# Optimization experiments

Hardware: AMD Instinct MI355X
Metric: run time of the kernel (lower is better)

The kernel has to match this reference:

```python
import jax, jax.numpy as jnp
import numpy as np

N = 50000
E = 500000
D = 128      # input_nf = output_nf = hidden_nf
EPS = 1e-8
MAX_TRANS = 10.0


def setup_inputs() -> dict:
    key = jax.random.key(0)
    ks = jax.random.split(key, 16)
    s = lambda k, shp: jax.random.normal(k, shp, dtype=jnp.float32) * 0.05
    inp = {
        "h": jax.random.normal(ks[0], (N, D), dtype=jnp.float32),
        "edge_index": jax.random.randint(ks[1], (2, E), 0, N, dtype=jnp.int64),
        "coord": jax.random.normal(ks[2], (N, 3), dtype=jnp.float32),
        # edge_mlp: Linear(2D+1 -> D), SiLU, Linear(D -> D), SiLU
        "We1": s(ks[3], (2 * D + 1, D)), "be1": jnp.zeros((D,), jnp.float32),
        "We2": s(ks[4], (D, D)),         "be2": jnp.zeros((D,), jnp.float32),
        # att_mlp: Linear(D -> 1), Sigmoid
        "Watt": s(ks[5], (D, 1)), "batt": jnp.zeros((1,), jnp.float32),
        # coord_mlp: Linear(D -> D), SiLU, Linear(D -> 1, bias=False, xavier gain=0.001)
        "Wc1": s(ks[6], (D, D)), "bc1": jnp.zeros((D,), jnp.float32),
        "Wc2": s(ks[7], (D, 1)) * 0.001,
        # node_mlp: Linear(2D -> D), SiLU, Linear(D -> D)
        "Wn1": s(ks[8], (2 * D, D)), "bn1": jnp.zeros((D,), jnp.float32),
        "Wn2": s(ks[9], (D, D)),     "bn2": jnp.zeros((D,), jnp.float32),
    }
    return inp


def _segment_mean(data, seg_ids, num_segments):
    tot = jax.ops.segment_sum(data, seg_ids, num_segments=num_segments)
    cnt = jax.ops.segment_sum(jnp.ones_like(data), seg_ids, num_segments=num_segments)
    return tot / jnp.clip(cnt, 1.0, None)


def reference(h, edge_index, coord, We1, be1, We2, be2, Watt, batt,
              Wc1, bc1, Wc2, Wn1, bn1, Wn2, bn2):
    row, col = edge_index[0], edge_index[1]

    # coord2radial (normalize=False)
    coord_diff = coord[row] - coord[col]                      # [E, 3]
    radial = jnp.sum(coord_diff ** 2, axis=1, keepdims=True)  # [E, 1]

    # edge_model with attention
    e_in = jnp.concatenate([h[row], h[col], radial], axis=1)  # [E, 2D+1]
    e = jax.nn.silu(e_in @ We1 + be1)
    edge_feat = jax.nn.silu(e @ We2 + be2)                    # [E, D]
    att = jax.nn.sigmoid(edge_feat @ Watt + batt)             # [E, 1]
    edge_feat = edge_feat * att

    # coord_model (update_coords=True, coords_agg='mean', tanh=False)
    cw = jax.nn.silu(edge_feat @ Wc1 + bc1) @ Wc2             # [E, 1]
    trans = jnp.clip(coord_diff * cw, -MAX_TRANS, MAX_TRANS)  # [E, 3]
    agg_c = jnp.clip(_segment_mean(trans, row, N), -MAX_TRANS, MAX_TRANS)
    coord_out = coord + agg_c

    # node_model (residual=True)
    agg = jax.ops.segment_sum(edge_feat, row, num_segments=N)  # [N, D]
    n_in = jnp.concatenate([h, agg], axis=1)                   # [N, 2D]
    h_out = h + (jax.nn.silu(n_in @ Wn1 + bn1) @ Wn2 + bn2)

    return h_out, coord_out, edge_feat
```

## Files before the change

### kernel.cpp

```cpp
#include <hip/hip_runtime.h>

typedef unsigned short ushort_t;
typedef __attribute__((ext_vector_type(8))) short short8;
typedef __attribute__((ext_vector_type(4))) short short4v;
typedef __attribute__((ext_vector_type(4))) float f32x4;

#define NN 50000
#define EE 500000
#define DD 128
#define MAXT 10.0f

#define MFMA(a,b,c) __builtin_amdgcn_mfma_f32_16x16x32_bf16((a),(b),(c),0,0,0)

__device__ __forceinline__ ushort_t f2bf(float x){
  unsigned u = __float_as_uint(x);
  u += 0x7FFFu + ((u>>16)&1u);
  return (ushort_t)(u>>16);
}
__device__ __forceinline__ float sigm(float x){ return 1.0f/(1.0f+__expf(-x)); }
__device__ __forceinline__ float siluf(float x){ return x*sigm(x); }
__device__ __forceinline__ float clamp10(float x){ return fminf(fmaxf(x,-MAXT),MAXT); }

__global__ void k_prep(const float* __restrict__ We1, const float* __restrict__ We2,
                       const float* __restrict__ Wc1, const float* __restrict__ Wn1,
                       const float* __restrict__ Wn2, ushort_t* __restrict__ wpre)
{
  int idx = blockIdx.x*256 + threadIdx.x;
  if (idx >= 7*16384) return;
  int mat = idx >> 14;
  int loc = idx & 16383;
  int n = loc >> 7;
  int kidx = loc & 127;
  int ko = 16*(kidx&7) + (kidx>>3);
  float v;
  switch(mat){
    case 0: v = We1[kidx*DD + n]; break;
    case 1: v = We1[(128+kidx)*DD + n]; break;
    case 2: v = We2[ko*DD + n]; break;
    case 3: v = Wc1[ko*DD + n]; break;
    case 4: v = Wn1[kidx*DD + n]; break;
    case 5: v = Wn1[(128+kidx)*DD + n]; break;
    default: v = Wn2[ko*DD + n]; break;
  }
  int byteoff = n*256 + ((kidx*2) ^ ((n&7)<<4));
  *(ushort_t*)((char*)wpre + (size_t)mat*32768 + byteoff) = f2bf(v);
}

__global__ void k_hprep(const float* __restrict__ h, ushort_t* __restrict__ hb)
{
  int i = blockIdx.x*256 + threadIdx.x;
  if (i >= NN*DD/8) return;
  f32x4 x = ((const f32x4*)h)[2*i];
  f32x4 y = ((const f32x4*)h)[2*i+1];
  short8 t;
  #pragma unroll
  for (int j=0;j<4;++j){ t[j]=(short)f2bf(x[j]); t[j+4]=(short)f2bf(y[j]); }
  ((short8*)hb)[i] = t;
}

__global__ void k_zero(int* __restrict__ cnt){
  int i = blockIdx.x*256 + threadIdx.x;
  if (i < NN) cnt[i] = 0;
}
__global__ void k_count(const int* __restrict__ eidx, int* __restrict__ cnt){
  int e = blockIdx.x*256 + threadIdx.x;
  if (e < EE) atomicAdd(&cnt[eidx[e]], 1);
}
#define SCAN_B 196
__global__ void k_bsum(const int* __restrict__ cnt, int* __restrict__ bsum){
  __shared__ int sh[256];
  int t = threadIdx.x;
  int i = blockIdx.x*256 + t;
  sh[t] = (i < NN) ? cnt[i] : 0;
  __syncthreads();
  for (int off=128; off>0; off>>=1){
    if (t < off) sh[t] += sh[t+off];
    __syncthreads();
  }
  if (t==0) bsum[blockIdx.x] = sh[0];
}
__global__ void k_bscan(const int* __restrict__ bsum, int* __restrict__ boff){
  __shared__ int sh[256];
  int t = threadIdx.x;
  sh[t] = (t < SCAN_B) ? bsum[t] : 0;
  __syncthreads();
  for (int off=1; off<256; off<<=1){
    int x = (t>=off) ? sh[t-off] : 0;
    __syncthreads();
    sh[t] += x;
    __syncthreads();
  }
  if (t < SCAN_B) boff[t] = (t>0) ? sh[t-1] : 0;
}
__global__ void k_rscan(const int* __restrict__ cnt, const int* __restrict__ boff,
                        int* __restrict__ rowstart, int* __restrict__ cursor){
  __shared__ int sh[256];
  int t = threadIdx.x;
  int i = blockIdx.x*256 + t;
  int v = (i < NN) ? cnt[i] : 0;
  sh[t] = v;
  __syncthreads();
  for (int off=1; off<256; off<<=1){
    int x = (t>=off) ? sh[t-off] : 0;
    __syncthreads();
    sh[t] += x;
    __syncthreads();
  }
  int excl = sh[t] - v + boff[blockIdx.x];
  if (i < NN){ rowstart[i] = excl; cursor[i] = excl; }
  if (i == 0) rowstart[NN] = EE;
}
__global__ void k_scatter(const int* __restrict__ eidx, int* __restrict__ cursor,
                          int* __restrict__ csr){
  int e = blockIdx.x*256 + threadIdx.x;
  if (e < EE){
    int p = atomicAdd(&cursor[eidx[e]], 1);
    csr[p] = e;
  }
}

__device__ __forceinline__ void stage(const ushort_t* __restrict__ wpre, int mat,
                                      ushort_t* Wbuf, int tid)
{
  const f32x4* src = (const f32x4*)(wpre + (size_t)mat*16384);
  f32x4* dst = (f32x4*)Wbuf;
  #pragma unroll
  for (int i=0;i<4;++i) dst[tid + 512*i] = src[tid + 512*i];
}
__device__ __forceinline__ void zacc(f32x4 acc[2][4]){
  #pragma unroll
  for (int i=0;i<2;++i)
    #pragma unroll
    for (int j=0;j<4;++j) acc[i][j] = (f32x4){0.f,0.f,0.f,0.f};
}
__device__ __forceinline__ void gemm_b16(const short8 af[2][4], const ushort_t* Wbuf,
                                         int cbase, int q, int s, f32x4 acc[2][4])
{
  #pragma unroll
  for (int kc=0;kc<4;++kc){
    const int koff = ((kc*64+q*16) ^ ((s&7)<<4));
    #pragma unroll
    for (int ct=0;ct<4;++ct){
      short8 bf = *(const short8*)((const char*)Wbuf + (cbase+ct*16+s)*256 + koff);
      acc[0][ct] = MFMA(af[0][kc],bf,acc[0][ct]);
      acc[1][ct] = MFMA(af[1][kc],bf,acc[1][ct]);
    }
  }
}
__device__ __forceinline__ void gemm_lds16(const ushort_t* ebuf, const ushort_t* Wbuf,
                                           int mbase, int cbase, int q, int s,
                                           f32x4 acc[2][4])
{
  #pragma unroll
  for (int kc=0;kc<4;++kc){
    const int koff = ((kc*64+q*16) ^ ((s&7)<<4));
    short8 a0 = *(const short8*)((const char*)ebuf + (mbase+s)*256 + koff);
    short8 a1 = *(const short8*)((const char*)ebuf + (mbase+16+s)*256 + koff);
    #pragma unroll
    for (int ct=0;ct<4;++ct){
      short8 bf = *(const short8*)((const char*)Wbuf + (cbase+ct*16+s)*256 + koff);
      acc[0][ct] = MFMA(a0,bf,acc[0][ct]);
      acc[1][ct] = MFMA(a1,bf,acc[1][ct]);
    }
  }
}

__launch_bounds__(512,4)
__global__ void k_edge(const ushort_t* __restrict__ hb,
                       const int* __restrict__ eidx,
                       const float* __restrict__ coord,
                       const float* __restrict__ We1,
                       const float* __restrict__ be1,
                       const float* __restrict__ be2,
                       const float* __restrict__ Watt,
                       const float* __restrict__ batt,
                       const float* __restrict__ bc1,
                       const float* __restrict__ Wc2,
                       const ushort_t* __restrict__ wpre,
                       float* __restrict__ ef_out,
                       float* __restrict__ trans)
{
  __shared__ ushort_t Wbuf[16384];
  __shared__ ushort_t ebuf[16384];
  __shared__ float dscr[128][2];
  const int tid = threadIdx.x;
  const int wv = tid>>6, ln = tid&63;
  const int wm = wv&3, wn = wv>>2;
  const int q = ln>>4, s = ln&15;
  const int cbase = wn*64;
  const int we0 = blockIdx.x*128;
  const int mb = wm*32;
  const int* rowI = eidx;
  const int* colI = eidx + EE;

  const int eM = min(we0 + mb + (ln&31), EE-1);
  const int rM = rowI[eM], cM = colI[eM];
  const float cdx = coord[rM*3+0]-coord[cM*3+0];
  const float cdy = coord[rM*3+1]-coord[cM*3+1];
  const float cdz = coord[rM*3+2]-coord[cM*3+2];
  const float radial = cdx*cdx+cdy*cdy+cdz*cdz;

  const int eS0 = min(we0 + mb + s,      EE-1);
  const int eS1 = min(we0 + mb + 16 + s, EE-1);
  const int nR0 = rowI[eS0], nR1 = rowI[eS1];
  const int nC0 = colI[eS0], nC1 = colI[eS1];

  f32x4 acc[2][4];
  short8 af[2][4];
  zacc(acc);

  #pragma unroll
  for (int kc=0;kc<4;++kc){
    af[0][kc] = *(const short8*)(hb + (size_t)nR0*DD + kc*32 + q*8);
    af[1][kc] = *(const short8*)(hb + (size_t)nR1*DD + kc*32 + q*8);
  }
  stage(wpre, 0, Wbuf, tid);
  __syncthreads();
  gemm_b16(af, Wbuf, cbase, q, s, acc);

  #pragma unroll
  for (int kc=0;kc<4;++kc){
    af[0][kc] = *(const short8*)(hb + (size_t)nC0*DD + kc*32 + q*8);
    af[1][kc] = *(const short8*)(hb + (size_t)nC1*DD + kc*32 + q*8);
  }
  __syncthreads();
  stage(wpre, 1, Wbuf, tid);
  __syncthreads();
  gemm_b16(af, Wbuf, cbase, q, s, acc);

  {
    float wr[4], bb[4];
    #pragma unroll
    for (int ct=0;ct<4;++ct){ wr[ct]=We1[256*DD + cbase+16*ct+s]; bb[ct]=be1[cbase+16*ct+s]; }
    #pragma unroll
    for (int mt=0;mt<2;++mt){
      #pragma unroll
      for (int r=0;r<4;++r){
        int mloc = mt*16 + q*4 + r;
        float rad = __shfl(radial, mloc);
        short4v pk;
        #pragma unroll
        for (int ct=0;ct<4;++ct) pk[ct]=(short)f2bf(siluf(acc[mt][ct][r] + rad*wr[ct] + bb[ct]));
        int m = mb + mloc;
        *(short4v*)((char*)ebuf + m*256 + ((16*s+8*wn) ^ ((m&7)<<4))) = pk;
      }
    }
  }
  zacc(acc);
  __syncthreads();
  stage(wpre, 2, Wbuf, tid);
  __syncthreads();

  gemm_lds16(ebuf, Wbuf, mb, cbase, q, s, acc);
  {
    float wa[4], bb[4];
    #pragma unroll
    for (int ct=0;ct<4;++ct){ wa[ct]=Watt[cbase+16*ct+s]; bb[ct]=be2[cbase+16*ct+s]; }
    #pragma unroll
    for (int mt=0;mt<2;++mt){
      #pragma unroll
      for (int r=0;r<4;++r){
        float p = 0.f;
        #pragma unroll
        for (int ct=0;ct<4;++ct){
          float v = siluf(acc[mt][ct][r] + bb[ct]);
          acc[mt][ct][r] = v;
          p += v*wa[ct];
        }
        p += __shfl_xor(p,1); p += __shfl_xor(p,2);
        p += __shfl_xor(p,4); p += __shfl_xor(p,8);
        if (s==0) dscr[mb + mt*16 + q*4 + r][wn] = p;
      }
    }
  }
  __syncthreads();
  stage(wpre, 3, Wbuf, tid);
  {
    const float bat = batt[0];
    #pragma unroll
    for (int mt=0;mt<2;++mt){
      #pragma unroll
      for (int r=0;r<4;++r){
        int m = mb + mt*16 + q*4 + r;
        float att = sigm(dscr[m][0] + dscr[m][1] + bat);
        short4v pk;
        #pragma unroll
        for (int ct=0;ct<4;++ct){
          acc[mt][ct][r] *= att;
          pk[ct]=(short)f2bf(acc[mt][ct][r]);
        }
        *(short4v*)((char*)ebuf + m*256 + ((16*s+8*wn) ^ ((m&7)<<4))) = pk;
        int e = we0 + m;
        if (e < EE){
          float* rp = ef_out + (size_t)e*DD + cbase + s;
          #pragma unroll
          for (int ct=0;ct<4;++ct) rp[16*ct] = acc[mt][ct][r];
        }
      }
    }
  }
  zacc(acc);
  __syncthreads();

  gemm_lds16(ebuf, Wbuf, mb, cbase, q, s, acc);
  {
    float wc[4], bb[4];
    #pragma unroll
    for (int ct=0;ct<4;++ct){ wc[ct]=Wc2[cbase+16*ct+s]; bb[ct]=bc1[cbase+16*ct+s]; }
    #pragma unroll
    for (int mt=0;mt<2;++mt){
      #pragma unroll
      for (int r=0;r<4;++r){
        float p = 0.f;
        #pragma unroll
        for (int ct=0;ct<4;++ct) p += siluf(acc[mt][ct][r]+bb[ct])*wc[ct];
        p += __shfl_xor(p,1); p += __shfl_xor(p,2);
        p += __shfl_xor(p,4); p += __shfl_xor(p,8);
        if (s==0) dscr[mb + mt*16 + q*4 + r][wn] = p;
      }
    }
  }
  __syncthreads();
  if (wn==0 && ln<32){
    int e = we0 + mb + ln;
    if (e < EE){
      float p = dscr[mb+ln][0] + dscr[mb+ln][1];
      trans[(size_t)e*3+0] = clamp10(cdx*p);
      trans[(size_t)e*3+1] = clamp10(cdy*p);
      trans[(size_t)e*3+2] = clamp10(cdz*p);
    }
  }
}

__launch_bounds__(256)
__global__ void k_agg(const float* __restrict__ ef,
                      const float* __restrict__ trans,
                      const int* __restrict__ rowstart,
                      const int* __restrict__ csr,
                      const float* __restrict__ coord,
                      ushort_t* __restrict__ aggb,
                      float* __restrict__ coord_out)
{
  const int wv = threadIdx.x>>6, ln = threadIdx.x&63;
  const int n = blockIdx.x*4 + wv;
  if (n >= NN) return;
  const int rs = rowstart[n], re = rowstart[n+1];
  const int deg = re - rs;
  const int half = ln>>5, l4 = (ln&31)*4;
  float a0=0,a1=0,a2=0,a3=0;
  for (int j=half; j<deg; j+=2){
    const float* p = ef + (size_t)csr[rs+j]*DD + l4;
    f32x4 v = *(const f32x4*)p;
    a0+=v[0]; a1+=v[1]; a2+=v[2]; a3+=v[3];
  }
  a0 += __shfl_xor(a0,32); a1 += __shfl_xor(a1,32);
  a2 += __shfl_xor(a2,32); a3 += __shfl_xor(a3,32);
  if (half==0){
    short4v o = { (short)f2bf(a0),(short)f2bf(a1),(short)f2bf(a2),(short)f2bf(a3) };
    *(short4v*)(aggb + (size_t)n*DD + l4) = o;
  }
  float tx=0,ty=0,tz=0;
  for (int j=ln;j<deg;j+=64){
    const float* t = trans + (size_t)csr[rs+j]*3;
    tx+=t[0]; ty+=t[1]; tz+=t[2];
  }
  #pragma unroll
  for (int m=1;m<64;m<<=1){
    tx+=__shfl_xor(tx,m); ty+=__shfl_xor(ty,m); tz+=__shfl_xor(tz,m);
  }
  if (ln==0){
    const float inv = 1.0f/(float)max(deg,1);
    coord_out[(size_t)n*3+0] = coord[(size_t)n*3+0] + clamp10(tx*inv);
    coord_out[(size_t)n*3+1] = coord[(size_t)n*3+1] + clamp10(ty*inv);
    coord_out[(size_t)n*3+2] = coord[(size_t)n*3+2] + clamp10(tz*inv);
  }
}

__launch_bounds__(512,4)
__global__ void k_node(const float* __restrict__ h,
                       const ushort_t* __restrict__ hb,
                       const ushort_t* __restrict__ aggb,
                       const ushort_t* __restrict__ wpre,
                       const float* __restrict__ bn1,
                       const float* __restrict__ bn2,
                       float* __restrict__ hout)
{
  __shared__ ushort_t Wbuf[16384];
  __shared__ ushort_t ubuf[16384];
  const int tid = threadIdx.x;
  const int wv = tid>>6, ln = tid&63;
  const int wm = wv&3, wn = wv>>2;
  const int q = ln>>4, s = ln&15;
  const int cbase = wn*64;
  const int n0 = blockIdx.x*128;
  const int mb = wm*32;
  const int nd0 = min(n0 + mb + s,      NN-1);
  const int nd1 = min(n0 + mb + 16 + s, NN-1);

  f32x4 acc[2][4];
  short8 af[2][4];
  zacc(acc);

  #pragma unroll
  for (int kc=0;kc<4;++kc){
    af[0][kc] = *(const short8*)(hb + (size_t)nd0*DD + kc*32 + q*8);
    af[1][kc] = *(const short8*)(hb + (size_t)nd1*DD + kc*32 + q*8);
  }
  stage(wpre, 4, Wbuf, tid);
  __syncthreads();
  gemm_b16(af, Wbuf, cbase, q, s, acc);

  #pragma unroll
  for (int kc=0;kc<4;++kc){
    af[0][kc] = *(const short8*)(aggb + (size_t)nd0*DD + kc*32 + q*8);
    af[1][kc] = *(const short8*)(aggb + (size_t)nd1*DD + kc*32 + q*8);
  }
  __syncthreads();
  stage(wpre, 5, Wbuf, tid);
  __syncthreads();
  gemm_b16(af, Wbuf, cbase, q, s, acc);

  {
    float bb[4];
    #pragma unroll
    for (int ct=0;ct<4;++ct) bb[ct]=bn1[cbase+16*ct+s];
    #pragma unroll
    for (int mt=0;mt<2;++mt){
      #pragma unroll
      for (int r=0;r<4;++r){
        int m = mb + mt*16 + q*4 + r;
        short4v pk;
        #pragma unroll
        for (int ct=0;ct<4;++ct) pk[ct]=(short)f2bf(siluf(acc[mt][ct][r]+bb[ct]));
        *(short4v*)((char*)ubuf + m*256 + ((16*s+8*wn) ^ ((m&7)<<4))) = pk;
      }
    }
  }
  zacc(acc);
  __syncthreads();
  stage(wpre, 6, Wbuf, tid);
  __syncthreads();

  gemm_lds16(ubuf, Wbuf, mb, cbase, q, s, acc);

  {
    float bb[4];
    #pragma unroll
    for (int ct=0;ct<4;++ct) bb[ct]=bn2[cbase+16*ct+s];
    #pragma unroll
    for (int mt=0;mt<2;++mt){
      #pragma unroll
      for (int r=0;r<4;++r){
        int n = n0 + mb + mt*16 + q*4 + r;
        if (n < NN){
          const float* hp = h + (size_t)n*DD + cbase + s;
          float* op = hout + (size_t)n*DD + cbase + s;
          #pragma unroll
          for (int ct=0;ct<4;++ct) op[16*ct] = hp[16*ct] + acc[mt][ct][r] + bb[ct];
        }
      }
    }
  }
}

extern "C" void kernel_launch(void* const* d_in, const int* in_sizes, int n_in,
                              void* d_out, int out_size, void* d_ws, size_t ws_size,
                              hipStream_t stream)
{
  const float* h    = (const float*)d_in[0];
  const int*   eidx = (const int*)  d_in[1];
  const float* coord= (const float*)d_in[2];
  const float* We1  = (const float*)d_in[3];
  const float* be1  = (const float*)d_in[4];
  const float* We2  = (const float*)d_in[5];
  const float* be2  = (const float*)d_in[6];
  const float* Watt = (const float*)d_in[7];
  const float* batt = (const float*)d_in[8];
  const float* Wc1  = (const float*)d_in[9];
  const float* bc1  = (const float*)d_in[10];
  const float* Wc2  = (const float*)d_in[11];
  const float* Wn1  = (const float*)d_in[12];
  const float* bn1  = (const float*)d_in[13];
  const float* Wn2  = (const float*)d_in[14];
  const float* bn2  = (const float*)d_in[15];

  float* hout     = (float*)d_out;
  float* coordout = hout + (size_t)NN*DD;
  float* efout    = coordout + (size_t)NN*3;

  char* ws = (char*)d_ws;
  float*    trans = (float*)(ws);
  ushort_t* aggb  = (ushort_t*)(ws + 6000000);
  ushort_t* hb    = (ushort_t*)(ws + 18800000);
  int*   cnt     = (int*)  (ws + 31600000);
  int*   cursor  = (int*)  (ws + 31800000);
  int*   rowstart= (int*)  (ws + 32000000);
  int*   csr     = (int*)  (ws + 32200064);
  ushort_t* wpre = (ushort_t*)(ws + 34200064);
  int*   bsum    = csr;
  int*   boff    = csr + 256;

  k_prep   <<<448, 256, 0, stream>>>(We1, We2, Wc1, Wn1, Wn2, wpre);
  k_hprep  <<<3125,256, 0, stream>>>(h, hb);
  k_zero   <<<196, 256, 0, stream>>>(cnt);
  k_count  <<<1954,256, 0, stream>>>(eidx, cnt);
  k_bsum   <<<196, 256, 0, stream>>>(cnt, bsum);
  k_bscan  <<<1,   256, 0, stream>>>(bsum, boff);
  k_rscan  <<<196, 256, 0, stream>>>(cnt, boff, rowstart, cursor);
  k_scatter<<<1954,256, 0, stream>>>(eidx, cursor, csr);
  k_edge   <<<3907,512, 0, stream>>>(hb, eidx, coord, We1, be1, be2, Watt, batt,
                                     bc1, Wc2, wpre, efout, trans);
  k_agg    <<<12500,256,0, stream>>>(efout, trans, rowstart, csr, coord, aggb, coordout);
  k_node   <<<391, 512, 0, stream>>>(h, hb, aggb, wpre, bn1, bn2, hout);
}
```

Before: 655.0 us.

## Precompute per-node first-layer projections and process edges in CSR order

Splits the first edge-MLP layer by linearity: a new kernel computes h@We1_top+be1 and h@We1_bottom once per node into fp32 buffers, and the edge kernel gathers and adds these rows instead of running two 128x128 GEMMs per edge. Edges are now processed in row-sorted CSR order so trans is written contiguously, and k_agg reads it without indirection. The edge features are scattered back to their original edge positions. This trades edge-level MFMA work for larger fp32 gathers (512B per node per operand) and two extra 25MB intermediate buffers. The We2 prep layout changes to match the new LDS write pattern for ebuf.

After: 699.2 us. 1.07x slower.

```diff
diff --git a/kernel.cpp b/kernel.cpp
--- a/kernel.cpp
+++ b/kernel.cpp
@@ -36,7 +36,7 @@
   switch(mat){
     case 0: v = We1[kidx*DD + n]; break;
     case 1: v = We1[(128+kidx)*DD + n]; break;
-    case 2: v = We2[ko*DD + n]; break;
+    case 2: v = We2[kidx*DD + n]; break;
     case 3: v = Wc1[ko*DD + n]; break;
     case 4: v = Wn1[kidx*DD + n]; break;
     case 5: v = Wn1[(128+kidx)*DD + n]; break;
@@ -166,11 +166,76 @@
 }
 
 __launch_bounds__(512,4)
-__global__ void k_edge(const ushort_t* __restrict__ hb,
+__global__ void k_pre1(const ushort_t* __restrict__ hb,
+                       const ushort_t* __restrict__ wpre,
+                       const float* __restrict__ be1,
+                       float* __restrict__ H1a, float* __restrict__ H1b)
+{
+  __shared__ ushort_t Wbuf[16384];
+  const int tid = threadIdx.x;
+  const int wv = tid>>6, ln = tid&63;
+  const int wm = wv&3, wn = wv>>2;
+  const int q = ln>>4, s = ln&15;
+  const int cbase = wn*64;
+  const int n0 = blockIdx.x*128;
+  const int mb = wm*32;
+  const int nd0 = min(n0 + mb + s,      NN-1);
+  const int nd1 = min(n0 + mb + 16 + s, NN-1);
+
+  f32x4 acc[2][4];
+  short8 af[2][4];
+  zacc(acc);
+  #pragma unroll
+  for (int kc=0;kc<4;++kc){
+    af[0][kc] = *(const short8*)(hb + (size_t)nd0*DD + kc*32 + q*8);
+    af[1][kc] = *(const short8*)(hb + (size_t)nd1*DD + kc*32 + q*8);
+  }
+  stage(wpre, 0, Wbuf, tid);
+  __syncthreads();
+  gemm_b16(af, Wbuf, cbase, q, s, acc);
+  {
+    float bb[4];
+    #pragma unroll
+    for (int ct=0;ct<4;++ct) bb[ct]=be1[cbase+16*ct+s];
+    #pragma unroll
+    for (int mt=0;mt<2;++mt)
+      #pragma unroll
+      for (int r=0;r<4;++r){
+        int n = n0 + mb + mt*16 + q*4 + r;
+        if (n < NN){
+          float* op = H1a + (size_t)n*DD + cbase + s;
+          #pragma unroll
+          for (int ct=0;ct<4;++ct) op[16*ct] = acc[mt][ct][r] + bb[ct];
+        }
+      }
+  }
+  zacc(acc);
+  __syncthreads();
+  stage(wpre, 1, Wbuf, tid);
+  __syncthreads();
+  gemm_b16(af, Wbuf, cbase, q, s, acc);
+  {
+    #pragma unroll
+    for (int mt=0;mt<2;++mt)
+      #pragma unroll
+      for (int r=0;r<4;++r){
+        int n = n0 + mb + mt*16 + q*4 + r;
+        if (n < NN){
+          float* op = H1b + (size_t)n*DD + cbase + s;
+          #pragma unroll
+          for (int ct=0;ct<4;++ct) op[16*ct] = acc[mt][ct][r];
+        }
+      }
+  }
+}
+
+__launch_bounds__(512,4)
+__global__ void k_edge(const float* __restrict__ H1a,
+                       const float* __restrict__ H1b,
                        const int* __restrict__ eidx,
+                       const int* __restrict__ csr,
                        const float* __restrict__ coord,
                        const float* __restrict__ We1,
-                       const float* __restrict__ be1,
                        const float* __restrict__ be2,
                        const float* __restrict__ Watt,
                        const float* __restrict__ batt,
@@ -188,67 +253,56 @@
   const int wm = wv&3, wn = wv>>2;
   const int q = ln>>4, s = ln&15;
   const int cbase = wn*64;
-  const int we0 = blockIdx.x*128;
+  const int eb0 = blockIdx.x*128;
   const int mb = wm*32;
   const int* rowI = eidx;
   const int* colI = eidx + EE;
 
-  const int eM = min(we0 + mb + (ln&31), EE-1);
-  const int rM = rowI[eM], cM = colI[eM];
-  const float cdx = coord[rM*3+0]-coord[cM*3+0];
-  const float cdy = coord[rM*3+1]-coord[cM*3+1];
-  const float cdz = coord[rM*3+2]-coord[cM*3+2];
-  const float radial = cdx*cdx+cdy*cdy+cdz*cdz;
-
-  const int eS0 = min(we0 + mb + s,      EE-1);
-  const int eS1 = min(we0 + mb + 16 + s, EE-1);
-  const int nR0 = rowI[eS0], nR1 = rowI[eS1];
-  const int nC0 = colI[eS0], nC1 = colI[eS1];
+  const int jg = eb0 + mb + (ln&31);
+  const int og = csr[min(jg, EE-1)];
+  const int rg = rowI[og], cg = colI[og];
+  const float cdx = coord[rg*3+0]-coord[cg*3+0];
+  const float cdy = coord[rg*3+1]-coord[cg*3+1];
+  const float cdz = coord[rg*3+2]-coord[cg*3+2];
+
+  const int o0 = csr[min(eb0+mb+s,    EE-1)];
+  const int o1 = csr[min(eb0+mb+16+s, EE-1)];
+  const int r0 = rowI[o0], c0 = colI[o0];
+  const int r1 = rowI[o1], c1 = colI[o1];
+  float rad[2];
+  { float dx=coord[r0*3+0]-coord[c0*3+0], dy=coord[r0*3+1]-coord[c0*3+1],
+          dz=coord[r0*3+2]-coord[c0*3+2];
+    rad[0]=dx*dx+dy*dy+dz*dz; }
+  { float dx=coord[r1*3+0]-coord[c1*3+0], dy=coord[r1*3+1]-coord[c1*3+1],
+          dz=coord[r1*3+2]-coord[c1*3+2];
+    rad[1]=dx*dx+dy*dy+dz*dz; }
+
+  stage(wpre, 2, Wbuf, tid);
+
+  #pragma unroll
+  for (int mt=0; mt<2; ++mt){
+    const int nR = mt ? r1 : r0, nC = mt ? c1 : c0;
+    const float rd = rad[mt];
+    const int m = mb + mt*16 + s;
+    #pragma unroll
+    for (int gi=0; gi<2; ++gi){
+      const int g = wn*8 + q*2 + gi;
+      const f32x4* pa = (const f32x4*)(H1a + (size_t)nR*DD + g*8);
+      const f32x4* pb = (const f32x4*)(H1b + (size_t)nC*DD + g*8);
+      const f32x4* pw = (const f32x4*)(We1 + 256*DD + g*8);
+      f32x4 a0=pa[0], a1=pa[1], bv0=pb[0], bv1=pb[1], w0=pw[0], w1=pw[1];
+      short8 pk;
+      #pragma unroll
+      for (int t=0;t<4;++t){
+        pk[t]   = (short)f2bf(siluf(a0[t]+bv0[t]+rd*w0[t]));
+        pk[t+4] = (short)f2bf(siluf(a1[t]+bv1[t]+rd*w1[t]));
+      }
+      *(short8*)((char*)ebuf + m*256 + ((g*16) ^ ((m&7)<<4))) = pk;
+    }
+  }
 
   f32x4 acc[2][4];
-  short8 af[2][4];
   zacc(acc);
-
-  #pragma unroll
-  for (int kc=0;kc<4;++kc){
-    af[0][kc] = *(const short8*)(hb + (size_t)nR0*DD + kc*32 + q*8);
-    af[1][kc] = *(const short8*)(hb + (size_t)nR1*DD + kc*32 + q*8);
-  }
-  stage(wpre, 0, Wbuf, tid);
-  __syncthreads();
-  gemm_b16(af, Wbuf, cbase, q, s, acc);
-
-  #pragma unroll
-  for (int kc=0;kc<4;++kc){
-    af[0][kc] = *(const short8*)(hb + (size_t)nC0*DD + kc*32 + q*8);
-    af[1][kc] = *(const short8*)(hb + (size_t)nC1*DD + kc*32 + q*8);
-  }
-  __syncthreads();
-  stage(wpre, 1, Wbuf, tid);
-  __syncthreads();
-  gemm_b16(af, Wbuf, cbase, q, s, acc);
-
-  {
-    float wr[4], bb[4];
-    #pragma unroll
-    for (int ct=0;ct<4;++ct){ wr[ct]=We1[256*DD + cbase+16*ct+s]; bb[ct]=be1[cbase+16*ct+s]; }
-    #pragma unroll
-    for (int mt=0;mt<2;++mt){
-      #pragma unroll
-      for (int r=0;r<4;++r){
-        int mloc = mt*16 + q*4 + r;
-        float rad = __shfl(radial, mloc);
-        short4v pk;
-        #pragma unroll
-        for (int ct=0;ct<4;++ct) pk[ct]=(short)f2bf(siluf(acc[mt][ct][r] + rad*wr[ct] + bb[ct]));
-        int m = mb + mloc;
-        *(short4v*)((char*)ebuf + m*256 + ((16*s+8*wn) ^ ((m&7)<<4))) = pk;
-      }
-    }
-  }
-  zacc(acc);
-  __syncthreads();
-  stage(wpre, 2, Wbuf, tid);
   __syncthreads();
 
   gemm_lds16(ebuf, Wbuf, mb, cbase, q, s, acc);
@@ -290,9 +344,9 @@
           pk[ct]=(short)f2bf(acc[mt][ct][r]);
         }
         *(short4v*)((char*)ebuf + m*256 + ((16*s+8*wn) ^ ((m&7)<<4))) = pk;
-        int e = we0 + m;
-        if (e < EE){
-          float* rp = ef_out + (size_t)e*DD + cbase + s;
+        int js = eb0 + m;
+        if (js < EE){
+          float* rp = ef_out + (size_t)csr[js]*DD + cbase + s;
           #pragma unroll
           for (int ct=0;ct<4;++ct) rp[16*ct] = acc[mt][ct][r];
         }
@@ -321,14 +375,11 @@
     }
   }
   __syncthreads();
-  if (wn==0 && ln<32){
-    int e = we0 + mb + ln;
-    if (e < EE){
-      float p = dscr[mb+ln][0] + dscr[mb+ln][1];
-      trans[(size_t)e*3+0] = clamp10(cdx*p);
-      trans[(size_t)e*3+1] = clamp10(cdy*p);
-      trans[(size_t)e*3+2] = clamp10(cdz*p);
-    }
+  if (wn==0 && ln<32 && jg < EE){
+    float p = dscr[mb+ln][0] + dscr[mb+ln][1];
+    trans[(size_t)jg*3+0] = clamp10(cdx*p);
+    trans[(size_t)jg*3+1] = clamp10(cdy*p);
+    trans[(size_t)jg*3+2] = clamp10(cdz*p);
   }
 }
 
@@ -361,7 +412,7 @@
   }
   float tx=0,ty=0,tz=0;
   for (int j=ln;j<deg;j+=64){
-    const float* t = trans + (size_t)csr[rs+j]*3;
+    const float* t = trans + (size_t)(rs+j)*3;
     tx+=t[0]; ty+=t[1]; tz+=t[2];
   }
   #pragma unroll
@@ -497,6 +548,8 @@
   int*   rowstart= (int*)  (ws + 32000000);
   int*   csr     = (int*)  (ws + 32200064);
   ushort_t* wpre = (ushort_t*)(ws + 34200064);
+  float* H1a     = (float*)(ws + 34429440);
+  float* H1b     = (float*)(ws + 60029440);
   int*   bsum    = csr;
   int*   boff    = csr + 256;
 
@@ -508,8 +561,9 @@
   k_bscan  <<<1,   256, 0, stream>>>(bsum, boff);
   k_rscan  <<<196, 256, 0, stream>>>(cnt, boff, rowstart, cursor);
   k_scatter<<<1954,256, 0, stream>>>(eidx, cursor, csr);
-  k_edge   <<<3907,512, 0, stream>>>(hb, eidx, coord, We1, be1, be2, Watt, batt,
-                                     bc1, Wc2, wpre, efout, trans);
+  k_pre1   <<<391, 512, 0, stream>>>(hb, wpre, be1, H1a, H1b);
+  k_edge   <<<3907,512, 0, stream>>>(H1a, H1b, eidx, csr, coord, We1, be2, Watt,
+                                     batt, bc1, Wc2, wpre, efout, trans);
   k_agg    <<<12500,256,0, stream>>>(efout, trans, rowstart, csr, coord, aggb, coordout);
   k_node   <<<391, 512, 0, stream>>>(h, hb, aggb, wpre, bn1, bn2, hout);
 }
```
